# Performance work log

Measured on AMD Instinct MI355X. Metric: run time of the kernel, lower is better.

Reference implementation:

```python
import jax, jax.numpy as jnp
import numpy as np

TEMPERATURE = 0.1
K = 5  # hard-coded k=5 in ANDCriterion.forward
EPS = 1e-12  # F.normalize eps


def setup_inputs() -> dict:
    key = jax.random.key(0)
    z = jax.random.normal(key, (8192, 1024), dtype=jnp.float32)
    return {"z": z}


def _normalize(z):
    nrm = jnp.sqrt(jnp.sum(z * z, axis=1, keepdims=True))
    return z / jnp.maximum(nrm, EPS)


def reference(z):
    n = z.shape[0]
    zn = _normalize(z)                      # [N, d], L2-normalized rows
    sim = zn @ zn.T                         # [N, N] cosine similarity
    # kNN neighbors (exclude self, which is always the top-1 hit)
    _, idx = jax.lax.top_k(sim, K + 1)      # [N, K+1]
    neigh = idx[:, 1:]                      # [N, K]
    # AND loss: softmax over non-self entries at temperature T;
    # loss_i = -log sum_{j in N(i)} p_ij
    logits = sim / TEMPERATURE
    logits = jnp.where(jnp.eye(n, dtype=bool), -jnp.inf, logits)
    logp = jax.nn.log_softmax(logits, axis=1)           # [N, N]
    neigh_logp = jnp.take_along_axis(logp, neigh, axis=1)  # [N, K]
    loss = -jnp.mean(jax.nn.logsumexp(neigh_logp, axis=1))
    return loss
```

## Files before the change

### kernel.cpp

```cpp
#include <hip/hip_runtime.h>
#include <stdint.h>

#define N_ROWS 8192
#define D_DIM  1024
#define NEG_BIG -1e30f
#define NCHUNK 16
#define CHUNK_J 512
#define NTILE 16
#define BUFSZ 17408

typedef __attribute__((ext_vector_type(16))) float f32x16;
typedef __attribute__((ext_vector_type(8)))  int   i32x8;
typedef __attribute__((ext_vector_type(4)))  int   i32x4;
typedef __attribute__((ext_vector_type(2)))  long  long2_t;

#define EXPC 14.4269504089f
#define EXPRAW(dst, v) { float _a = fmaf((v), EXPC, -EXPC);                 \
    asm("v_exp_f32 %0, %1" : "=v"(dst) : "v"(_a)); }

#define INS5(b0,b1,b2,b3,b4,v) {                        \
    float _n4 = __builtin_amdgcn_fmed3f(b3, (v), b4);   \
    float _n3 = __builtin_amdgcn_fmed3f(b2, (v), b3);   \
    float _n2 = __builtin_amdgcn_fmed3f(b1, (v), b2);   \
    float _n1 = __builtin_amdgcn_fmed3f(b0, (v), b1);   \
    b0 = fmaxf(b0, (v)); b1 = _n1; b2 = _n2; b3 = _n3; b4 = _n4; }

static __device__ inline uint32_t enc4(float x, float inv) {
    float q = fabsf(x) * inv;
    uint32_t n = q < 0.25f ? 0u : (q < 0.75f ? 1u : (q < 1.25f ? 2u : (q < 1.75f ? 3u :
                 (q < 2.5f  ? 4u : (q < 3.5f  ? 5u : (q < 5.0f  ? 6u : 7u))))));
    return n | (x < 0.f ? 8u : 0u);
}

__global__ __launch_bounds__(256) void norm_kernel(const float* __restrict__ z,
                                                   uint8_t* __restrict__ zn4,
                                                   uint8_t* __restrict__ sbq) {
    int wave = threadIdx.x >> 6;
    int lane = threadIdx.x & 63;
    int row  = blockIdx.x * 4 + wave;
    const float* zr = z + (size_t)row * D_DIM;
    float4 c[4];
    float ss = 0.f;
#pragma unroll
    for (int i = 0; i < 4; ++i) {
        c[i] = *(const float4*)(zr + i * 256 + lane * 4);
        ss += c[i].x*c[i].x + c[i].y*c[i].y + c[i].z*c[i].z + c[i].w*c[i].w;
    }
#pragma unroll
    for (int m = 1; m < 64; m <<= 1) ss += __shfl_xor(ss, m);
    float scale = 1.0f / fmaxf(sqrtf(ss), 1e-12f);
    const int J = row >> 5, r31 = row & 31;
    uint8_t* db = zn4 + (size_t)J * 16384;
    uint8_t* sb = sbq + (size_t)J * 1024;
#pragma unroll
    for (int i = 0; i < 4; ++i) {
        float x0 = c[i].x*scale, x1 = c[i].y*scale, x2 = c[i].z*scale, x3 = c[i].w*scale;
        float am = fmaxf(fmaxf(fabsf(x0), fabsf(x1)), fmaxf(fabsf(x2), fabsf(x3)));
        am = fmaxf(am, __shfl_xor(am, 1));
        am = fmaxf(am, __shfl_xor(am, 2));
        am = fmaxf(am, __shfl_xor(am, 4));
        uint32_t ub = __float_as_uint(am);
        int sbyte = (int)(ub >> 23) - 2 + (((ub & 0x7fffffu) > 0x400000u) ? 1 : 0);
        float inv = __uint_as_float((uint32_t)(254 - sbyte) << 23);
        uint32_t pk = enc4(x0, inv) | (enc4(x1, inv) << 4)
                    | (enc4(x2, inv) << 8) | (enc4(x3, inv) << 12);
        int m  = i * 4 + (lane >> 4);
        int l2 = r31 + 32 * ((lane >> 3) & 1);
        *(uint16_t*)(db + m * 1024 + l2 * 16 + 2 * (lane & 7)) = (uint16_t)pk;
        if ((lane & 7) == 0) {
            int j = lane >> 3;
            sb[(size_t)(r31 + 32 * (j & 1)) * 16 + i * 4 + (j >> 1)] = (uint8_t)sbyte;
        }
    }
}

__global__ __launch_bounds__(256, 2) void sim_kernel(const uint8_t* __restrict__ zn4,
                                                     const uint8_t* __restrict__ sbq,
                                                     float* __restrict__ pstats) {
    __shared__ __align__(16) char lds[2 * BUFSZ];
    const int tid  = threadIdx.x;
    const int w    = tid >> 6;
    const int l    = tid & 63;
    const int r32  = l & 31;
    const int h    = l >> 5;
    const int ib   = blockIdx.x >> 4;
    const int ch   = blockIdx.x & 15;
    const int j0c  = ch * CHUNK_J;
    const int i_lane = ib * 128 + w * 32 + r32;
    const int Ii   = ib * 4 + w;
    const int diag_jt = ((Ii >> 4) == ch) ? (Ii & 15) : -1;
    const char* ldsr = lds + l * 16;

#define GLL(SRC, DST) __builtin_amdgcn_global_load_lds(                         \
        (const __attribute__((address_space(1))) uint32_t*)(SRC),               \
        (__attribute__((address_space(3))) uint32_t*)(DST), 16, 0, 0)

#define STAGE(JTN, BUF) {                                                       \
        const uint8_t* sD_ = zn4 + (size_t)(ch * NTILE + (JTN)) * 16384;        \
        _Pragma("unroll")                                                       \
        for (int mm = 0; mm < 4; ++mm) {                                        \
            int m_ = w * 4 + mm;                                                \
            GLL(sD_ + m_ * 1024 + l * 16, (BUF) + m_ * 1024);                   \
        }                                                                       \
        if (w == 0)                                                             \
            GLL(sbq + (size_t)(ch * NTILE + (JTN)) * 1024 + l * 16,             \
                (BUF) + 16384);                                                 \
    }

    STAGE(0, lds);

    i32x8 bres8[8];
    {
        const uint8_t* rp = zn4 + (size_t)Ii * 16384 + l * 16;
#pragma unroll
        for (int g = 0; g < 8; ++g) {
            *(long2_t*)&bres8[g]       = *(const long2_t*)(rp + (2 * g) * 1024);
            *((long2_t*)&bres8[g] + 1) = *(const long2_t*)(rp + (2 * g + 1) * 1024);
        }
    }
    uint32_t sb_[4];
    {
        const uint32_t* sp = (const uint32_t*)(sbq + (size_t)Ii * 1024 + l * 16);
        sb_[0] = sp[0]; sb_[1] = sp[1]; sb_[2] = sp[2]; sb_[3] = sp[3];
    }

    float s0r = 0.f, s1r = 0.f;
    float b0 = NEG_BIG, b1 = NEG_BIG, b2 = NEG_BIG, b3 = NEG_BIG, b4 = NEG_BIG;
    f32x16 svp;
#pragma unroll
    for (int r = 0; r < 16; ++r) svp[r] = NEG_BIG;
    i32x8 areg0 = {0,0,0,0,0,0,0,0}, areg1 = {0,0,0,0,0,0,0,0};
    i32x8 btmp  = {0,0,0,0,0,0,0,0};

    __syncthreads();

#define EPI5() {                                                                \
        _Pragma("unroll")                                                       \
        for (int r = 0; r < 16; ++r) {                                          \
            float v = svp[r];                                                   \
            INS5(b0, b1, b2, b3, b4, v);                                        \
            float e_; EXPRAW(e_, v);                                            \
            if (r & 1) s1r += e_; else s0r += e_;                               \
        }                                                                       \
    }

#define MFMA_E(M) {                                                             \
        asm volatile("" : "+v"(bres8[(M) >> 1]));                               \
        *(long2_t*)&areg0 = *(const long2_t*)(ldst_ + (M) * 1024);              \
        acc0 = __builtin_amdgcn_mfma_scale_f32_32x32x64_f8f6f4(                 \
            areg0, bres8[(M) >> 1], acc0, 4, 4,                                 \
            (M) & 3, sa_[(M) >> 2], (M) & 3, sb_[(M) >> 2]); }
#define MFMA_O(M) {                                                             \
        *(long2_t*)&btmp  = *((const long2_t*)&bres8[(M) >> 1] + 1);            \
        *(long2_t*)&areg1 = *(const long2_t*)(ldst_ + (M) * 1024);              \
        acc1 = __builtin_amdgcn_mfma_scale_f32_32x32x64_f8f6f4(                 \
            areg1, btmp, acc1, 4, 4,                                            \
            (M) & 3, sa_[(M) >> 2], (M) & 3, sb_[(M) >> 2]); }

#define TILE_BODY(JT, CUR) {                                                    \
        if ((JT) + 1 < NTILE) STAGE((JT) + 1, lds + ((CUR) ^ BUFSZ));           \
        const char* ldst_ = ldsr + (CUR);                                       \
        uint32_t sa_[4];                                                        \
        {                                                                       \
            i32x4 sv = *(const i32x4*)(lds + (CUR) + 16384 + l * 16);           \
            sa_[0] = sv[0]; sa_[1] = sv[1]; sa_[2] = sv[2]; sa_[3] = sv[3];     \
        }                                                                       \
        f32x16 acc0, acc1;                                                      \
        _Pragma("unroll")                                                       \
        for (int r = 0; r < 16; ++r) { acc0[r] = 0.f; acc1[r] = 0.f; }          \
        __builtin_amdgcn_s_setprio(1);                                          \
        MFMA_E(0)  MFMA_O(1)  MFMA_E(2)  MFMA_O(3)                              \
        MFMA_E(4)  MFMA_O(5)  MFMA_E(6)  MFMA_O(7)                              \
        MFMA_E(8)  MFMA_O(9)  MFMA_E(10) MFMA_O(11)                             \
        MFMA_E(12) MFMA_O(13) MFMA_E(14) MFMA_O(15)                             \
        __builtin_amdgcn_s_setprio(0);                                          \
        EPI5();   \
        if ((JT) != diag_jt) {                                                  \
            _Pragma("unroll")                                                   \
            for (int r = 0; r < 16; ++r) svp[r] = acc0[r] + acc1[r];            \
        } else {                                                                \
            const int dd2 = i_lane - (j0c + (JT) * 32) - 4 * h;                 \
            _Pragma("unroll")                                                   \
            for (int r = 0; r < 16; ++r) {                                      \
                const int jm = (r & 3) + 8 * (r >> 2);                          \
                float v = acc0[r] + acc1[r];                                    \
                svp[r] = (dd2 == jm) ? NEG_BIG : v;                             \
            }                                                                   \
        }                                                                       \
        __syncthreads();                                                        \
    }

    for (int jt = 0; jt < NTILE; jt += 2) {
        TILE_BODY(jt, 0);
        TILE_BODY(jt + 1, BUFSZ);
    }
    EPI5();
#undef TILE_BODY
#undef MFMA_E
#undef MFMA_O
#undef EPI5
#undef STAGE
#undef GLL

    float s_run = s0r + s1r;
    s_run += __shfl_xor(s_run, 32);
    {
        float o0 = __shfl_xor(b0, 32), o1 = __shfl_xor(b1, 32), o2 = __shfl_xor(b2, 32),
              o3 = __shfl_xor(b3, 32), o4 = __shfl_xor(b4, 32);
        INS5(b0, b1, b2, b3, b4, o0); INS5(b0, b1, b2, b3, b4, o1);
        INS5(b0, b1, b2, b3, b4, o2); INS5(b0, b1, b2, b3, b4, o3);
        INS5(b0, b1, b2, b3, b4, o4);
    }
    if (h == 0) {
        float* p = pstats + ((size_t)ch * N_ROWS + i_lane) * 8;
        p[0] = s_run; p[1] = b0; p[2] = b1; p[3] = b2; p[4] = b3; p[5] = b4;
        p[6] = 0.f; p[7] = 0.f;
    }
}

__global__ __launch_bounds__(128) void reduce1(const float* __restrict__ pstats,
                                               float* __restrict__ partial) {
    int row = blockIdx.x * 128 + threadIdx.x;
    float S = 0.f;
    float b0 = NEG_BIG, b1 = NEG_BIG, b2 = NEG_BIG, b3 = NEG_BIG, b4 = NEG_BIG;
#pragma unroll
    for (int c = 0; c < NCHUNK; ++c) {
        const float* p = pstats + ((size_t)c * N_ROWS + row) * 8;
        S += p[0];
        float v0 = p[1], v1 = p[2], v2 = p[3], v3 = p[4], v4 = p[5];
        INS5(b0, b1, b2, b3, b4, v0); INS5(b0, b1, b2, b3, b4, v1);
        INS5(b0, b1, b2, b3, b4, v2); INS5(b0, b1, b2, b3, b4, v3);
        INS5(b0, b1, b2, b3, b4, v4);
    }
    float e0, e1, e2, e3, e4;
    EXPRAW(e0, b0); EXPRAW(e1, b1); EXPRAW(e2, b2); EXPRAW(e3, b3); EXPRAW(e4, b4);
    float S5 = e0 + e1 + e2 + e3 + e4;
    float loss = __logf(S) - __logf(S5);
#pragma unroll
    for (int m = 1; m < 64; m <<= 1) loss += __shfl_xor(loss, m);
    __shared__ float rr[2];
    if ((threadIdx.x & 63) == 0) rr[threadIdx.x >> 6] = loss;
    __syncthreads();
    if (threadIdx.x == 0) partial[blockIdx.x] = rr[0] + rr[1];
}

__global__ void reduce2(const float* __restrict__ partial, float* __restrict__ out) {
    float v = partial[threadIdx.x];
#pragma unroll
    for (int m = 1; m < 64; m <<= 1) v += __shfl_xor(v, m);
    if (threadIdx.x == 0) out[0] = v * (1.0f / N_ROWS);
}

extern "C" void kernel_launch(void* const* d_in, const int* in_sizes, int n_in,
                              void* d_out, int out_size, void* d_ws, size_t ws_size,
                              hipStream_t stream) {
    const float* z = (const float*)d_in[0];
    float* out = (float*)d_out;
    uint8_t* zn4   = (uint8_t*)d_ws;
    uint8_t* sbq   = (uint8_t*)d_ws + (size_t)4 * 1024 * 1024;
    float* pstats  = (float*)((char*)d_ws + (size_t)4608 * 1024);
    float* partial = (float*)((char*)d_ws + (size_t)13 * 1024 * 1024);

    norm_kernel<<<N_ROWS / 4, 256, 0, stream>>>(z, zn4, sbq);
    sim_kernel<<<64 * NCHUNK, 256, 0, stream>>>(zn4, sbq, pstats);
    reduce1<<<N_ROWS / 128, 128, 0, stream>>>(pstats, partial);
    reduce2<<<1, 64, 0, stream>>>(partial, out);
}
```

Baseline: 69.83 us.

## Split sim kernel into MFMA producer and epilogue consumer warp groups

```diff
diff --git a/kernel.cpp b/kernel.cpp
--- a/kernel.cpp
+++ b/kernel.cpp
@@ -7,9 +7,9 @@
 #define NCHUNK 16
 #define CHUNK_J 512
 #define NTILE 16
-#define BUFSZ 17408
 
 typedef __attribute__((ext_vector_type(16))) float f32x16;
+typedef __attribute__((ext_vector_type(4)))  float f32x4;
 typedef __attribute__((ext_vector_type(8)))  int   i32x8;
 typedef __attribute__((ext_vector_type(4)))  int   i32x4;
 typedef __attribute__((ext_vector_type(2)))  long  long2_t;
@@ -64,9 +64,12 @@
         float inv = __uint_as_float((uint32_t)(254 - sbyte) << 23);
         uint32_t pk = enc4(x0, inv) | (enc4(x1, inv) << 4)
                     | (enc4(x2, inv) << 8) | (enc4(x3, inv) << 12);
+        uint32_t pko = __shfl_xor(pk, 1);
         int m  = i * 4 + (lane >> 4);
         int l2 = r31 + 32 * ((lane >> 3) & 1);
-        *(uint16_t*)(db + m * 1024 + l2 * 16 + 2 * (lane & 7)) = (uint16_t)pk;
+        if ((lane & 1) == 0)
+            *(uint32_t*)(db + m * 1024 + l2 * 16 + 4 * ((lane & 7) >> 1))
+                = pk | (pko << 16);
         if ((lane & 7) == 0) {
             int j = lane >> 3;
             sb[(size_t)(r31 + 32 * (j & 1)) * 16 + i * 4 + (j >> 1)] = (uint8_t)sbyte;
@@ -74,10 +77,11 @@
     }
 }
 
-__global__ __launch_bounds__(256, 2) void sim_kernel(const uint8_t* __restrict__ zn4,
+__global__ __launch_bounds__(512, 2) void sim_kernel(const uint8_t* __restrict__ zn4,
                                                      const uint8_t* __restrict__ sbq,
                                                      float* __restrict__ pstats) {
-    __shared__ __align__(16) char lds[2 * BUFSZ];
+    __shared__ __align__(16) char Abuf[2][16384];
+    __shared__ __align__(16) char Pbuf[2][4][4096];
     const int tid  = threadIdx.x;
     const int w    = tid >> 6;
     const int l    = tid & 63;
@@ -86,136 +90,161 @@
     const int ib   = blockIdx.x >> 4;
     const int ch   = blockIdx.x & 15;
     const int j0c  = ch * CHUNK_J;
-    const int i_lane = ib * 128 + w * 32 + r32;
-    const int Ii   = ib * 4 + w;
+    const bool prod = (w < 4);
+    const int wp   = w & 3;
+    const int Ii   = ib * 4 + wp;
+    const int i_lane  = Ii * 32 + r32;
     const int diag_jt = ((Ii >> 4) == ch) ? (Ii & 15) : -1;
-    const char* ldsr = lds + l * 16;
 
 #define GLL(SRC, DST) __builtin_amdgcn_global_load_lds(                         \
         (const __attribute__((address_space(1))) uint32_t*)(SRC),               \
         (__attribute__((address_space(3))) uint32_t*)(DST), 16, 0, 0)
 
-#define STAGE(JTN, BUF) {                                                       \
-        const uint8_t* sD_ = zn4 + (size_t)(ch * NTILE + (JTN)) * 16384;        \
-        _Pragma("unroll")                                                       \
-        for (int mm = 0; mm < 4; ++mm) {                                        \
-            int m_ = w * 4 + mm;                                                \
-            GLL(sD_ + m_ * 1024 + l * 16, (BUF) + m_ * 1024);                   \
-        }                                                                       \
-        if (w == 0)                                                             \
-            GLL(sbq + (size_t)(ch * NTILE + (JTN)) * 1024 + l * 16,             \
-                (BUF) + 16384);                                                 \
-    }
-
-    STAGE(0, lds);
-
     i32x8 bres8[8];
-    {
+    uint32_t sw_[4];
+    i32x4 sa_v;
+    float s0r = 0.f, s1r = 0.f;
+    float b0 = NEG_BIG, b1 = NEG_BIG, b2 = NEG_BIG, b3 = NEG_BIG, b4 = NEG_BIG;
+
+    if (prod) {
         const uint8_t* rp = zn4 + (size_t)Ii * 16384 + l * 16;
 #pragma unroll
         for (int g = 0; g < 8; ++g) {
             *(long2_t*)&bres8[g]       = *(const long2_t*)(rp + (2 * g) * 1024);
             *((long2_t*)&bres8[g] + 1) = *(const long2_t*)(rp + (2 * g + 1) * 1024);
         }
-    }
-    uint32_t sb_[4];
-    {
         const uint32_t* sp = (const uint32_t*)(sbq + (size_t)Ii * 1024 + l * 16);
-        sb_[0] = sp[0]; sb_[1] = sp[1]; sb_[2] = sp[2]; sb_[3] = sp[3];
-    }
-
-    float s0r = 0.f, s1r = 0.f;
-    float b0 = NEG_BIG, b1 = NEG_BIG, b2 = NEG_BIG, b3 = NEG_BIG, b4 = NEG_BIG;
-    f32x16 svp;
-#pragma unroll
-    for (int r = 0; r < 16; ++r) svp[r] = NEG_BIG;
+        sw_[0] = sp[0]; sw_[1] = sp[1]; sw_[2] = sp[2]; sw_[3] = sp[3];
+        sa_v = *(const i32x4*)(sbq + (size_t)(ch * NTILE) * 1024 + l * 16);
+    } else {
+        const uint8_t* sD = zn4 + (size_t)(ch * NTILE) * 16384;
+#pragma unroll
+        for (int mm = 0; mm < 4; ++mm)
+            GLL(sD + (wp * 4 + mm) * 1024 + l * 16,
+                &Abuf[0][(wp * 4 + mm) * 1024]);
+        f32x4 ninf = {NEG_BIG, NEG_BIG, NEG_BIG, NEG_BIG};
+#pragma unroll
+        for (int rq = 0; rq < 4; ++rq)
+            *(f32x4*)(&Pbuf[1][wp][rq * 1024 + l * 16]) = ninf;
+    }
+
     i32x8 areg0 = {0,0,0,0,0,0,0,0}, areg1 = {0,0,0,0,0,0,0,0};
     i32x8 btmp  = {0,0,0,0,0,0,0,0};
 
     __syncthreads();
-
-#define EPI5() {                                                                \
-        _Pragma("unroll")                                                       \
-        for (int r = 0; r < 16; ++r) {                                          \
-            float v = svp[r];                                                   \
-            INS5(b0, b1, b2, b3, b4, v);                                        \
-            float e_; EXPRAW(e_, v);                                            \
-            if (r & 1) s1r += e_; else s0r += e_;                               \
-        }                                                                       \
-    }
 
 #define MFMA_E(M) {                                                             \
         asm volatile("" : "+v"(bres8[(M) >> 1]));                               \
         *(long2_t*)&areg0 = *(const long2_t*)(ldst_ + (M) * 1024);              \
         acc0 = __builtin_amdgcn_mfma_scale_f32_32x32x64_f8f6f4(                 \
             areg0, bres8[(M) >> 1], acc0, 4, 4,                                 \
-            (M) & 3, sa_[(M) >> 2], (M) & 3, sb_[(M) >> 2]); }
+            (M) & 3, sa_[(M) >> 2], (M) & 3, sw_[(M) >> 2]); }
 #define MFMA_O(M) {                                                             \
         *(long2_t*)&btmp  = *((const long2_t*)&bres8[(M) >> 1] + 1);            \
         *(long2_t*)&areg1 = *(const long2_t*)(ldst_ + (M) * 1024);              \
         acc1 = __builtin_amdgcn_mfma_scale_f32_32x32x64_f8f6f4(                 \
             areg1, btmp, acc1, 4, 4,                                            \
-            (M) & 3, sa_[(M) >> 2], (M) & 3, sb_[(M) >> 2]); }
-
-#define TILE_BODY(JT, CUR) {                                                    \
-        if ((JT) + 1 < NTILE) STAGE((JT) + 1, lds + ((CUR) ^ BUFSZ));           \
-        const char* ldst_ = ldsr + (CUR);                                       \
-        uint32_t sa_[4];                                                        \
-        {                                                                       \
-            i32x4 sv = *(const i32x4*)(lds + (CUR) + 16384 + l * 16);           \
-            sa_[0] = sv[0]; sa_[1] = sv[1]; sa_[2] = sv[2]; sa_[3] = sv[3];     \
-        }                                                                       \
-        f32x16 acc0, acc1;                                                      \
-        _Pragma("unroll")                                                       \
-        for (int r = 0; r < 16; ++r) { acc0[r] = 0.f; acc1[r] = 0.f; }          \
-        __builtin_amdgcn_s_setprio(1);                                          \
-        MFMA_E(0)  MFMA_O(1)  MFMA_E(2)  MFMA_O(3)                              \
-        MFMA_E(4)  MFMA_O(5)  MFMA_E(6)  MFMA_O(7)                              \
-        MFMA_E(8)  MFMA_O(9)  MFMA_E(10) MFMA_O(11)                             \
-        MFMA_E(12) MFMA_O(13) MFMA_E(14) MFMA_O(15)                             \
-        __builtin_amdgcn_s_setprio(0);                                          \
-        EPI5();   \
-        if ((JT) != diag_jt) {                                                  \
-            _Pragma("unroll")                                                   \
-            for (int r = 0; r < 16; ++r) svp[r] = acc0[r] + acc1[r];            \
-        } else {                                                                \
-            const int dd2 = i_lane - (j0c + (JT) * 32) - 4 * h;                 \
-            _Pragma("unroll")                                                   \
-            for (int r = 0; r < 16; ++r) {                                      \
-                const int jm = (r & 3) + 8 * (r >> 2);                          \
-                float v = acc0[r] + acc1[r];                                    \
-                svp[r] = (dd2 == jm) ? NEG_BIG : v;                             \
-            }                                                                   \
-        }                                                                       \
-        __syncthreads();                                                        \
-    }
-
-    for (int jt = 0; jt < NTILE; jt += 2) {
-        TILE_BODY(jt, 0);
-        TILE_BODY(jt + 1, BUFSZ);
-    }
-    EPI5();
-#undef TILE_BODY
-#undef MFMA_E
-#undef MFMA_O
-#undef EPI5
-#undef STAGE
-#undef GLL
-
-    float s_run = s0r + s1r;
-    s_run += __shfl_xor(s_run, 32);
-    {
+            (M) & 3, sa_[(M) >> 2], (M) & 3, sw_[(M) >> 2]); }
+
+    for (int t = 0; t < NTILE; ++t) {
+        if (prod) {
+            const char* ldst_ = &Abuf[t & 1][0] + l * 16;
+            uint32_t sa_[4];
+            sa_[0] = sa_v[0]; sa_[1] = sa_v[1]; sa_[2] = sa_v[2]; sa_[3] = sa_v[3];
+            if (t + 1 < NTILE)
+                sa_v = *(const i32x4*)(sbq + (size_t)(ch * NTILE + t + 1) * 1024
+                                       + l * 16);
+            f32x16 acc0, acc1;
+#pragma unroll
+            for (int r = 0; r < 16; ++r) { acc0[r] = 0.f; acc1[r] = 0.f; }
+            MFMA_E(0)  MFMA_O(1)  MFMA_E(2)  MFMA_O(3)
+            MFMA_E(4)  MFMA_O(5)  MFMA_E(6)  MFMA_O(7)
+            MFMA_E(8)  MFMA_O(9)  MFMA_E(10) MFMA_O(11)
+            MFMA_E(12) MFMA_O(13) MFMA_E(14) MFMA_O(15)
+            char* pw = &Pbuf[t & 1][wp][0] + l * 16;
+#pragma unroll
+            for (int rq = 0; rq < 4; ++rq) {
+                f32x4 vq;
+                vq[0] = acc0[rq * 4 + 0] + acc1[rq * 4 + 0];
+                vq[1] = acc0[rq * 4 + 1] + acc1[rq * 4 + 1];
+                vq[2] = acc0[rq * 4 + 2] + acc1[rq * 4 + 2];
+                vq[3] = acc0[rq * 4 + 3] + acc1[rq * 4 + 3];
+                *(f32x4*)(pw + rq * 1024) = vq;
+            }
+        } else {
+            if (t + 1 < NTILE) {
+                const uint8_t* sD = zn4 + (size_t)(ch * NTILE + t + 1) * 16384;
+#pragma unroll
+                for (int mm = 0; mm < 4; ++mm)
+                    GLL(sD + (wp * 4 + mm) * 1024 + l * 16,
+                        &Abuf[(t + 1) & 1][(wp * 4 + mm) * 1024]);
+            }
+            const char* pr = &Pbuf[(t + 1) & 1][wp][0] + l * 16;
+            f32x16 vv;
+#pragma unroll
+            for (int rq = 0; rq < 4; ++rq) {
+                f32x4 vq = *(const f32x4*)(pr + rq * 1024);
+                vv[rq * 4 + 0] = vq[0]; vv[rq * 4 + 1] = vq[1];
+                vv[rq * 4 + 2] = vq[2]; vv[rq * 4 + 3] = vq[3];
+            }
+            const int tm = t - 1;
+            if (tm == diag_jt) {
+                const int dd2 = i_lane - (j0c + tm * 32) - 4 * h;
+#pragma unroll
+                for (int r = 0; r < 16; ++r) {
+                    const int jm = (r & 3) + 8 * (r >> 2);
+                    if (dd2 == jm) vv[r] = NEG_BIG;
+                }
+            }
+#pragma unroll
+            for (int r = 0; r < 16; ++r) {
+                INS5(b0, b1, b2, b3, b4, vv[r]);
+                float e_; EXPRAW(e_, vv[r]);
+                if (r & 1) s1r += e_; else s0r += e_;
+            }
+        }
+        __syncthreads();
+    }
+
+    if (!prod) {
+        const char* pr = &Pbuf[1][wp][0] + l * 16;
+        f32x16 vv;
+#pragma unroll
+        for (int rq = 0; rq < 4; ++rq) {
+            f32x4 vq = *(const f32x4*)(pr + rq * 1024);
+            vv[rq * 4 + 0] = vq[0]; vv[rq * 4 + 1] = vq[1];
+            vv[rq * 4 + 2] = vq[2]; vv[rq * 4 + 3] = vq[3];
+        }
+        if (NTILE - 1 == diag_jt) {
+            const int dd2 = i_lane - (j0c + (NTILE - 1) * 32) - 4 * h;
+#pragma unroll
+            for (int r = 0; r < 16; ++r) {
+                const int jm = (r & 3) + 8 * (r >> 2);
+                if (dd2 == jm) vv[r] = NEG_BIG;
+            }
+        }
+#pragma unroll
+        for (int r = 0; r < 16; ++r) {
+            INS5(b0, b1, b2, b3, b4, vv[r]);
+            float e_; EXPRAW(e_, vv[r]);
+            if (r & 1) s1r += e_; else s0r += e_;
+        }
+        float s_run = s0r + s1r;
+        s_run += __shfl_xor(s_run, 32);
         float o0 = __shfl_xor(b0, 32), o1 = __shfl_xor(b1, 32), o2 = __shfl_xor(b2, 32),
               o3 = __shfl_xor(b3, 32), o4 = __shfl_xor(b4, 32);
         INS5(b0, b1, b2, b3, b4, o0); INS5(b0, b1, b2, b3, b4, o1);
         INS5(b0, b1, b2, b3, b4, o2); INS5(b0, b1, b2, b3, b4, o3);
         INS5(b0, b1, b2, b3, b4, o4);
-    }
-    if (h == 0) {
-        float* p = pstats + ((size_t)ch * N_ROWS + i_lane) * 8;
-        p[0] = s_run; p[1] = b0; p[2] = b1; p[3] = b2; p[4] = b3; p[5] = b4;
-        p[6] = 0.f; p[7] = 0.f;
-    }
+        if (h == 0) {
+            float* p = pstats + ((size_t)ch * N_ROWS + i_lane) * 8;
+            p[0] = s_run; p[1] = b0; p[2] = b1; p[3] = b2; p[4] = b3; p[5] = b4;
+            p[6] = 0.f; p[7] = 0.f;
+        }
+    }
+#undef MFMA_E
+#undef MFMA_O
+#undef GLL
 }
 
 __global__ __launch_bounds__(128) void reduce1(const float* __restrict__ pstats,
@@ -262,7 +291,7 @@
     float* partial = (float*)((char*)d_ws + (size_t)13 * 1024 * 1024);
 
     norm_kernel<<<N_ROWS / 4, 256, 0, stream>>>(z, zn4, sbq);
-    sim_kernel<<<64 * NCHUNK, 256, 0, stream>>>(zn4, sbq, pstats);
+    sim_kernel<<<64 * NCHUNK, 512, 0, stream>>>(zn4, sbq, pstats);
     reduce1<<<N_ROWS / 128, 128, 0, stream>>>(pstats, partial);
     reduce2<<<1, 64, 0, stream>>>(partial, out);
 }
```

New measurement: 74.27 us. +6.4%, slower.
